# Kernel optimization log

Hardware: AMD Instinct MI355X
Metric: run time of the kernel (lower is better)

Reference implementation:

```python
import jax, jax.numpy as jnp
import numpy as np
from jax import lax

KS = 3          # kernel_size
ITER = 24       # diffusion iterations
# itertools.product([0,1,-1], repeat=2) order from the torch source
OFFS = [(i, j) for i in (0, 1, -1) for j in (0, 1, -1)]


def setup_inputs() -> dict:
    key = jax.random.key(0)
    k1, k2, k3 = jax.random.split(key, 3)
    B, H, W = 8, 512, 512
    x = jax.random.normal(k1, (B, 1, H, W), jnp.float32)
    W_aff = jax.random.normal(k2, (KS * KS - 1, 1, KS, KS), jnp.float32) * 0.1
    b_aff = jax.random.normal(k3, (KS * KS - 1,), jnp.float32) * 0.1
    return {"x": x, "W_aff": W_aff, "b_aff": b_aff}


def _gen_kernel(aff):
    # aff: [B, 8, H, W] -> normalized 9-channel kernel [B, 9, H, W]
    abs_sum = jnp.sum(jnp.abs(aff), axis=1, keepdims=True)
    a = aff / abs_sum
    s = jnp.sum(a, axis=1, keepdims=True)
    return jnp.concatenate([1.0 - s, a], axis=1)


def reference(x, W_aff, b_aff):
    # affinity net: 1 -> 8 channel 3x3 SAME conv
    aff = lax.conv_general_dilated(x, W_aff, (1, 1), "SAME") + b_aff[None, :, None, None]
    kernel = _gen_kernel(aff)  # [B, 9, H, W]
    H, W = x.shape[2], x.shape[3]

    def body(_, xc):
        # zero-pad then take 9 shifted views: col_k[p] = x[p - off_k] (zero outside)
        xp = jnp.pad(xc, ((0, 0), (0, 0), (1, 1), (1, 1)))
        cols = jnp.concatenate(
            [xp[:, :, 1 - oi:1 - oi + H, 1 - oj:1 - oj + W] for (oi, oj) in OFFS],
            axis=1,
        )  # [B, 9, H, W]
        return jnp.sum(cols * kernel, axis=1, keepdims=True)

    return lax.fori_loop(0, ITER, body, x)
```

## Files before the change

### kernel.cpp

```cpp
#include <hip/hip_runtime.h>
#include <hip/hip_fp16.h>

constexpr int B = 8, H = 512, W = 512;
constexpr int N = B * H * W;
constexpr int HW = H * W;

constexpr int TT = 32;
constexpr int T  = 6;
constexpr int XR = TT + 2 * T;
constexpr int XE = XR * XR;
constexpr int NG = XR / 4;
constexpr int CR = XR - 2;
constexpr int NGT = CR * NG;
constexpr int NTH = H / TT, NTW = W / TT;
constexpr int NTILES = B * NTH * NTW;
constexpr int NT = 512;
constexpr int NF2 = XR * (XR / 2);

__global__ __launch_bounds__(256) void cspn_gen_kernel(
    const float* __restrict__ x, const float* __restrict__ Wa,
    const float* __restrict__ ba, __half* __restrict__ Kh) {
  int idx = blockIdx.x * 256 + threadIdx.x;
  if (idx >= N) return;
  int j = idx & (W - 1);
  int i = (idx >> 9) & (H - 1);
  const float* xb = x + (idx & ~(HW - 1));

  float v[9];
#pragma unroll
  for (int u = 0; u < 3; ++u) {
#pragma unroll
    for (int t = 0; t < 3; ++t) {
      int ii = i + u - 1, jj = j + t - 1;
      v[u * 3 + t] = (unsigned(ii) < (unsigned)H && unsigned(jj) < (unsigned)W)
                         ? xb[ii * W + jj]
                         : 0.0f;
    }
  }

  float aff[8];
  float abs_sum = 0.0f;
#pragma unroll
  for (int c = 0; c < 8; ++c) {
    float a = ba[c];
#pragma unroll
    for (int t = 0; t < 9; ++t) a += v[t] * Wa[c * 9 + t];
    aff[c] = a;
    abs_sum += fabsf(a);
  }
  float inv = 1.0f / abs_sum;
#pragma unroll
  for (int c = 0; c < 8; ++c) aff[c] *= inv;

  union { uint4 u; __half2 h[4]; } pk;
#pragma unroll
  for (int c = 0; c < 4; ++c)
    pk.h[c] = __floats2half2_rn(aff[2 * c], aff[2 * c + 1]);
  *reinterpret_cast<uint4*>(Kh + (size_t)idx * 8) = pk.u;
}

__device__ __forceinline__ float dpp_shr1(float v) {
  int r = __builtin_amdgcn_update_dpp(__float_as_int(v), __float_as_int(v),
                                      0x138, 0xF, 0xF, false);
  return __int_as_float(r);
}
__device__ __forceinline__ float dpp_shl1(float v) {
  int r = __builtin_amdgcn_update_dpp(__float_as_int(v), __float_as_int(v),
                                      0x130, 0xF, 0xF, false);
  return __int_as_float(r);
}

#define H2F(h) __half2float(h)

__global__ __launch_bounds__(NT, 6) void cspn_fused(
    const float* __restrict__ xin, const __half* __restrict__ Kh,
    float* __restrict__ xout) {
  __shared__ __align__(16) float sBuf[64 + 2 * XE + 64];
  float* sX = sBuf + 64;

  int bid = blockIdx.x;
  int wg = (bid & 7) * (NTILES / 8) + (bid >> 3);
  int b  = wg / (NTH * NTW);
  int rr = wg % (NTH * NTW);
  int ti0 = (rr / NTW) * TT, tj0 = (rr % NTW) * TT;
  int tid = threadIdx.x;
  int lane = tid & 63;

  bool active = tid < NGT;
  int xi  = 1 + tid / NG;
  int xj0 = (tid % NG) * 4;

  const float* xb = xin + (size_t)b * HW;

  int li0 = tid / (XR / 2), gc0 = tid - li0 * (XR / 2);
  int p1 = tid + NT;
  int li1 = p1 / (XR / 2), gc1 = p1 - li1 * (XR / 2);
  bool st1 = p1 < NF2;
  float2 sv0 = make_float2(0.f, 0.f), sv1 = make_float2(0.f, 0.f);
  {
    int gi = ti0 + li0 - T, gj = tj0 + 2 * gc0 - T;
    if ((unsigned)gi < (unsigned)H && (unsigned)gj < (unsigned)W)
      sv0 = *reinterpret_cast<const float2*>(xb + gi * W + gj);
  }
  if (st1) {
    int gi = ti0 + li1 - T, gj = tj0 + 2 * gc1 - T;
    if ((unsigned)gi < (unsigned)H && (unsigned)gj < (unsigned)W)
      sv1 = *reinterpret_cast<const float2*>(xb + gi * W + gj);
  }

  __half2 kh[4][4];
  float4 k0;
  {
    int gi  = ti0 + xi - T;
    int gj0 = tj0 + xj0 - T;
    bool rowv = active && (unsigned)gi < (unsigned)H;
    const __half* Kb =
        Kh + ((size_t)b * HW + (size_t)(rowv ? gi : 0) * W) * 8;
    float k0v[4];
#pragma unroll
    for (int p = 0; p < 4; ++p) {
      int gj = gj0 + p;
      union { uint4 u; __half2 h[4]; } pk;
      pk.u = make_uint4(0u, 0u, 0u, 0u);
      if (rowv && (unsigned)gj < (unsigned)W)
        pk.u = *reinterpret_cast<const uint4*>(Kb + (size_t)gj * 8);
      float2 f01 = __half22float2(pk.h[0]);
      float2 f23 = __half22float2(pk.h[1]);
      float2 f45 = __half22float2(pk.h[2]);
      float2 f67 = __half22float2(pk.h[3]);
      k0v[p] = 1.0f - (f01.x + f01.y + f23.x + f23.y +
                       f45.x + f45.y + f67.x + f67.y);
      kh[p][0] = pk.h[0]; kh[p][1] = pk.h[1];
      kh[p][2] = pk.h[2]; kh[p][3] = pk.h[3];
    }
    k0 = make_float4(k0v[0], k0v[1], k0v[2], k0v[3]);
  }

  *reinterpret_cast<float2*>(sX + li0 * XR + 2 * gc0) = sv0;
  if (st1) *reinterpret_cast<float2*>(sX + li1 * XR + 2 * gc1) = sv1;
  if (tid < 64) {
    sBuf[tid] = 0.f;
    sBuf[64 + 2 * XE + tid] = 0.f;
  }
  if (tid < 2 * XR) {
    int r = (tid < XR) ? 0 : (XR - 1);
    int c = (tid < XR) ? tid : tid - XR;
    sX[XE + r * XR + c] = 0.f;
  }
  __syncthreads();

  int base = xi * XR + xj0;
  float4 c1;
  if (active) c1 = *reinterpret_cast<const float4*>(sX + base);
#pragma unroll
  for (int s = 0; s < T; ++s) {
    const float* Xc = sX + (s & 1) * XE;
    float* Xn = sX + (((s & 1) ^ 1)) * XE;
    if (active) {
      float4 c0 = *reinterpret_cast<const float4*>(Xc + base - XR);
      float4 c2 = *reinterpret_cast<const float4*>(Xc + base + XR);
      float l0 = dpp_shr1(c0.w), l1 = dpp_shr1(c1.w), l2 = dpp_shr1(c2.w);
      float r0 = dpp_shl1(c0.x), r1 = dpp_shl1(c1.x), r2 = dpp_shl1(c2.x);
      if (lane == 0) {
        l0 = Xc[base - XR - 1];
        l1 = Xc[base - 1];
        l2 = Xc[base + XR - 1];
      }
      if (lane == 63) {
        r0 = Xc[base - XR + 4];
        r1 = Xc[base + 4];
        r2 = Xc[base + XR + 4];
      }
      float4 acc;
      acc.x = k0.x * c1.x
            + H2F(kh[0][0].x) * l1   + H2F(kh[0][0].y) * c1.y
            + H2F(kh[0][1].x) * c0.x + H2F(kh[0][1].y) * l0
            + H2F(kh[0][2].x) * c0.y + H2F(kh[0][2].y) * c2.x
            + H2F(kh[0][3].x) * l2   + H2F(kh[0][3].y) * c2.y;
      acc.y = k0.y * c1.y
            + H2F(kh[1][0].x) * c1.x + H2F(kh[1][0].y) * c1.z
            + H2F(kh[1][1].x) * c0.y + H2F(kh[1][1].y) * c0.x
            + H2F(kh[1][2].x) * c0.z + H2F(kh[1][2].y) * c2.y
            + H2F(kh[1][3].x) * c2.x + H2F(kh[1][3].y) * c2.z;
      acc.z = k0.z * c1.z
            + H2F(kh[2][0].x) * c1.y + H2F(kh[2][0].y) * c1.w
            + H2F(kh[2][1].x) * c0.z + H2F(kh[2][1].y) * c0.y
            + H2F(kh[2][2].x) * c0.w + H2F(kh[2][2].y) * c2.z
            + H2F(kh[2][3].x) * c2.y + H2F(kh[2][3].y) * c2.w;
      acc.w = k0.w * c1.w
            + H2F(kh[3][0].x) * c1.z + H2F(kh[3][0].y) * r1
            + H2F(kh[3][1].x) * c0.w + H2F(kh[3][1].y) * c0.z
            + H2F(kh[3][2].x) * r0   + H2F(kh[3][2].y) * c2.w
            + H2F(kh[3][3].x) * c2.z + H2F(kh[3][3].y) * r2;
      *reinterpret_cast<float4*>(Xn + base) = acc;
      c1 = acc;
    }
    __syncthreads();
  }

  float* yb = xout + (size_t)b * HW;
  int i  = tid >> 4;
  int pj = (tid & 15) * 2;
  float2 v = *reinterpret_cast<const float2*>(sX + (i + T) * XR + (pj + T));
  *reinterpret_cast<float2*>(yb + (size_t)(ti0 + i) * W + (tj0 + pj)) = v;
}

extern "C" void kernel_launch(void* const* d_in, const int* in_sizes, int n_in,
                              void* d_out, int out_size, void* d_ws,
                              size_t ws_size, hipStream_t stream) {
  const float* x  = (const float*)d_in[0];
  const float* Wa = (const float*)d_in[1];
  const float* ba = (const float*)d_in[2];
  float* out = (float*)d_out;

  __half* Kh = (__half*)d_ws;
  float* xa = (float*)d_ws + 4 * (size_t)N;
  cspn_gen_kernel<<<dim3(N / 256), dim3(256), 0, stream>>>(x, Wa, ba, Kh);

  const float* src = x;
  for (int l = 0; l < 24 / T; ++l) {
    float* dst = (l & 1) ? out : xa;
    cspn_fused<<<dim3(NTILES), dim3(NT), 0, stream>>>(src, Kh, dst);
    src = dst;
  }
}
```

Measured before the change: 111.1 us.

## Fuse affinity kernel generation into first diffusion pass via shared memory

Removes the separate affinity-generation kernel. The first fused diffusion launch now computes the normalized fp16 affinities for its haloed tile into shared memory, uses them directly, and writes the interior tile's affinities to global memory for the later passes. This saves one launch and the global reread of affinities in the first pass. In exchange, halo pixels are recomputed redundantly and the first launch needs extra shared memory (XE*16 bytes), which may reduce occupancy.

```diff
diff --git a/kernel.cpp b/kernel.cpp
--- a/kernel.cpp
+++ b/kernel.cpp
@@ -17,48 +17,6 @@
 constexpr int NT = 512;
 constexpr int NF2 = XR * (XR / 2);
 
-__global__ __launch_bounds__(256) void cspn_gen_kernel(
-    const float* __restrict__ x, const float* __restrict__ Wa,
-    const float* __restrict__ ba, __half* __restrict__ Kh) {
-  int idx = blockIdx.x * 256 + threadIdx.x;
-  if (idx >= N) return;
-  int j = idx & (W - 1);
-  int i = (idx >> 9) & (H - 1);
-  const float* xb = x + (idx & ~(HW - 1));
-
-  float v[9];
-#pragma unroll
-  for (int u = 0; u < 3; ++u) {
-#pragma unroll
-    for (int t = 0; t < 3; ++t) {
-      int ii = i + u - 1, jj = j + t - 1;
-      v[u * 3 + t] = (unsigned(ii) < (unsigned)H && unsigned(jj) < (unsigned)W)
-                         ? xb[ii * W + jj]
-                         : 0.0f;
-    }
-  }
-
-  float aff[8];
-  float abs_sum = 0.0f;
-#pragma unroll
-  for (int c = 0; c < 8; ++c) {
-    float a = ba[c];
-#pragma unroll
-    for (int t = 0; t < 9; ++t) a += v[t] * Wa[c * 9 + t];
-    aff[c] = a;
-    abs_sum += fabsf(a);
-  }
-  float inv = 1.0f / abs_sum;
-#pragma unroll
-  for (int c = 0; c < 8; ++c) aff[c] *= inv;
-
-  union { uint4 u; __half2 h[4]; } pk;
-#pragma unroll
-  for (int c = 0; c < 4; ++c)
-    pk.h[c] = __floats2half2_rn(aff[2 * c], aff[2 * c + 1]);
-  *reinterpret_cast<uint4*>(Kh + (size_t)idx * 8) = pk.u;
-}
-
 __device__ __forceinline__ float dpp_shr1(float v) {
   int r = __builtin_amdgcn_update_dpp(__float_as_int(v), __float_as_int(v),
                                       0x138, 0xF, 0xF, false);
@@ -72,10 +30,13 @@
 
 #define H2F(h) __half2float(h)
 
+template <int GENK>
 __global__ __launch_bounds__(NT, 6) void cspn_fused(
-    const float* __restrict__ xin, const __half* __restrict__ Kh,
-    float* __restrict__ xout) {
+    const float* __restrict__ x0, const float* __restrict__ Wa,
+    const float* __restrict__ ba, const float* __restrict__ xin,
+    __half* __restrict__ Kg, float* __restrict__ xout) {
   __shared__ __align__(16) float sBuf[64 + 2 * XE + 64];
+  __shared__ __align__(16) __half sK[GENK ? XE * 8 : 8];
   float* sX = sBuf + 64;
 
   int bid = blockIdx.x;
@@ -90,7 +51,8 @@
   int xi  = 1 + tid / NG;
   int xj0 = (tid % NG) * 4;
 
-  const float* xb = xin + (size_t)b * HW;
+  const float* xb  = xin + (size_t)b * HW;
+  const float* x0b = x0 + (size_t)b * HW;
 
   int li0 = tid / (XR / 2), gc0 = tid - li0 * (XR / 2);
   int p1 = tid + NT;
@@ -110,12 +72,13 @@
 
   __half2 kh[4][4];
   float4 k0;
-  {
+
+  if (!GENK) {
     int gi  = ti0 + xi - T;
     int gj0 = tj0 + xj0 - T;
     bool rowv = active && (unsigned)gi < (unsigned)H;
     const __half* Kb =
-        Kh + ((size_t)b * HW + (size_t)(rowv ? gi : 0) * W) * 8;
+        Kg + ((size_t)b * HW + (size_t)(rowv ? gi : 0) * W) * 8;
     float k0v[4];
 #pragma unroll
     for (int p = 0; p < 4; ++p) {
@@ -147,7 +110,69 @@
     int c = (tid < XR) ? tid : tid - XR;
     sX[XE + r * XR + c] = 0.f;
   }
+
+  if (GENK) {
+    for (int p = tid; p < XE; p += NT) {
+      int li = p / XR, lj = p - li * XR;
+      int gi = ti0 + li - T, gj = tj0 + lj - T;
+      union { uint4 u; __half2 h[4]; } pk;
+      pk.u = make_uint4(0u, 0u, 0u, 0u);
+      if ((unsigned)gi < (unsigned)H && (unsigned)gj < (unsigned)W) {
+        float v[9];
+#pragma unroll
+        for (int u = 0; u < 3; ++u) {
+#pragma unroll
+          for (int t = 0; t < 3; ++t) {
+            int ii = gi + u - 1, jj = gj + t - 1;
+            v[u * 3 + t] =
+                (unsigned(ii) < (unsigned)H && unsigned(jj) < (unsigned)W)
+                    ? x0b[ii * W + jj]
+                    : 0.0f;
+          }
+        }
+        float aff[8];
+        float abs_sum = 0.0f;
+#pragma unroll
+        for (int c = 0; c < 8; ++c) {
+          float a = ba[c];
+#pragma unroll
+          for (int t = 0; t < 9; ++t) a += v[t] * Wa[c * 9 + t];
+          aff[c] = a;
+          abs_sum += fabsf(a);
+        }
+        float inv = 1.0f / abs_sum;
+#pragma unroll
+        for (int c = 0; c < 8; ++c) aff[c] *= inv;
+#pragma unroll
+        for (int c = 0; c < 4; ++c)
+          pk.h[c] = __floats2half2_rn(aff[2 * c], aff[2 * c + 1]);
+      }
+      *reinterpret_cast<uint4*>(sK + (size_t)p * 8) = pk.u;
+      if ((unsigned)(li - T) < (unsigned)TT && (unsigned)(lj - T) < (unsigned)TT)
+        *reinterpret_cast<uint4*>(
+            Kg + ((size_t)b * HW + (size_t)gi * W + gj) * 8) = pk.u;
+    }
+  }
   __syncthreads();
+
+  if (GENK) {
+    int fb = active ? (xi * XR + xj0) : 0;
+    float k0v[4];
+#pragma unroll
+    for (int p = 0; p < 4; ++p) {
+      union { uint4 u; __half2 h[4]; } pk;
+      pk.u = *reinterpret_cast<const uint4*>(sK + (size_t)(fb + p) * 8);
+      float2 f01 = __half22float2(pk.h[0]);
+      float2 f23 = __half22float2(pk.h[1]);
+      float2 f45 = __half22float2(pk.h[2]);
+      float2 f67 = __half22float2(pk.h[3]);
+      k0v[p] = 1.0f - (f01.x + f01.y + f23.x + f23.y +
+                       f45.x + f45.y + f67.x + f67.y);
+      kh[p][0] = pk.h[0]; kh[p][1] = pk.h[1];
+      kh[p][2] = pk.h[2]; kh[p][3] = pk.h[3];
+    }
+    k0 = make_float4(k0v[0], k0v[1], k0v[2], k0v[3]);
+  }
 
   int base = xi * XR + xj0;
   float4 c1;
@@ -215,12 +240,13 @@
 
   __half* Kh = (__half*)d_ws;
   float* xa = (float*)d_ws + 4 * (size_t)N;
-  cspn_gen_kernel<<<dim3(N / 256), dim3(256), 0, stream>>>(x, Wa, ba, Kh);
-
-  const float* src = x;
-  for (int l = 0; l < 24 / T; ++l) {
+
+  cspn_fused<1><<<dim3(NTILES), dim3(NT), 0, stream>>>(x, Wa, ba, x, Kh, xa);
+  const float* src = xa;
+  for (int l = 1; l < 24 / T; ++l) {
     float* dst = (l & 1) ? out : xa;
-    cspn_fused<<<dim3(NTILES), dim3(NT), 0, stream>>>(src, Kh, dst);
+    cspn_fused<0><<<dim3(NTILES), dim3(NT), 0, stream>>>(x, Wa, ba, src, Kh,
+                                                         dst);
     src = dst;
   }
 }
```

Result: slower. 116.4 us (+4.8%).
